# Kernel optimization log

Hardware: AMD Instinct MI355X
Metric: run time of the kernel (lower is better)

The kernel has to match this reference:

```python
import jax, jax.numpy as jnp
import numpy as np

N = 100000
E = 1600000
G = 64  # number of graphs
H = 128
BN_EPS = 1e-5


def setup_inputs() -> dict:
    key = jax.random.key(0)
    ks = jax.random.split(key, 12)
    x = jax.random.normal(ks[0], (N, 3), dtype=jnp.float32)
    edge_index = jax.random.randint(ks[1], (2, E), 0, N, dtype=jnp.int64)
    batch = jnp.sort(jax.random.randint(ks[2], (N,), 0, G, dtype=jnp.int64))
    W1 = jax.random.normal(ks[3], (3, H), dtype=jnp.float32) * 0.3
    W2 = jax.random.normal(ks[4], (H, H), dtype=jnp.float32) * 0.05
    W3 = jax.random.normal(ks[5], (H, H), dtype=jnp.float32) * 0.05
    lin_W = jax.random.normal(ks[6], (H, 2), dtype=jnp.float32) * 0.05
    d = {
        'x': x, 'edge_index': edge_index, 'batch': batch,
        'W1': W1, 'b1': jnp.zeros((H,), jnp.float32),
        'W2': W2, 'b2': jnp.zeros((H,), jnp.float32),
        'W3': W3, 'b3': jnp.zeros((H,), jnp.float32),
        'lin_W': lin_W, 'lin_b': jnp.zeros((2,), jnp.float32),
    }
    for i, kk in zip((1, 2, 3), ks[7:10]):
        d[f'bn{i}_g'] = jnp.ones((H,), jnp.float32)
        d[f'bn{i}_b'] = jnp.zeros((H,), jnp.float32)
        d[f'bn{i}_m'] = jnp.zeros((H,), jnp.float32)
        d[f'bn{i}_v'] = jax.random.uniform(kk, (H,), dtype=jnp.float32, minval=0.5, maxval=1.5)
    return d


def _gcn(x, src, dst, norm, W, b):
    # GCNConv: out = scatter_add(norm * (xW)[src], dst) + b
    h = x @ W
    msg = h[src] * norm[:, None]
    agg = jax.ops.segment_sum(msg, dst, num_segments=N)
    return agg + b


def _bn_eval(x, g, b, m, v):
    return (x - m) * jax.lax.rsqrt(v + BN_EPS) * g + b


def reference(x, edge_index, batch, W1, b1, W2, b2, W3, b3,
              bn1_g, bn1_b, bn1_m, bn1_v,
              bn2_g, bn2_b, bn2_m, bn2_v,
              bn3_g, bn3_b, bn3_m, bn3_v,
              lin_W, lin_b):
    loop = jnp.arange(N, dtype=edge_index.dtype)
    src = jnp.concatenate([edge_index[0], loop])
    dst = jnp.concatenate([edge_index[1], loop])
    # symmetric normalization with self-loops: deg from destination nodes
    deg = jax.ops.segment_sum(jnp.ones_like(dst, dtype=x.dtype), dst, num_segments=N)
    dinv = jnp.where(deg > 0, jax.lax.rsqrt(deg), 0.0)
    norm = dinv[src] * dinv[dst]

    h = jax.nn.relu(_bn_eval(_gcn(x, src, dst, norm, W1, b1), bn1_g, bn1_b, bn1_m, bn1_v))
    h = jax.nn.relu(_bn_eval(_gcn(h, src, dst, norm, W2, b2), bn2_g, bn2_b, bn2_m, bn2_v))
    h = jax.nn.relu(_bn_eval(_gcn(h, src, dst, norm, W3, b3), bn3_g, bn3_b, bn3_m, bn3_v))
    # dropout is identity in eval mode
    sums = jax.ops.segment_sum(h, batch, num_segments=G)
    cnts = jax.ops.segment_sum(jnp.ones((N,), h.dtype), batch, num_segments=G)
    pooled = sums / jnp.maximum(cnts, 1.0)[:, None]
    return pooled @ lin_W + lin_b
```

## Files before the change

### kernel.cpp

```cpp
#include <hip/hip_runtime.h>

#define NN 100000
#define EE 1600000
#define GG 64
#define HH 128
#define BN_EPS 1e-5f

#define CB 782
#define NB 256
#define TILE 6250

typedef unsigned short ushort_t;
typedef __attribute__((ext_vector_type(8))) short bf16x8;
typedef __attribute__((ext_vector_type(4))) float f32x4;

#define MFMA16 __builtin_amdgcn_mfma_f32_16x16x32_bf16

#define WFRAG_LO 16384

static __device__ inline ushort_t f2bf(float f) {
    unsigned u = __float_as_uint(f);
    unsigned r = (u + 0x7FFF + ((u >> 16) & 1)) >> 16;
    return (ushort_t)r;
}
static __device__ inline float bf2f(ushort_t b) {
    return __uint_as_float(((unsigned)b) << 16);
}


__global__ __launch_bounds__(256) void k_hist(const int* __restrict__ ei,
                                              int* __restrict__ histG) {
    __shared__ int h[CB];
    int t = threadIdx.x;
    for (int i = t; i < CB; i += 256) h[i] = 0;
    __syncthreads();
    int e0 = blockIdx.x * TILE;
    for (int i = t; i < TILE; i += 256) {
        int d = ei[EE + e0 + i];
        atomicAdd(&h[d >> 7], 1);
    }
    __syncthreads();
    for (int i = t; i < CB; i += 256) histG[blockIdx.x * CB + i] = h[i];
}

__global__ __launch_bounds__(NB) void k_bscan(int* __restrict__ histG,
                                              int* __restrict__ total) {
    __shared__ int sh[NB];
    int t = threadIdx.x;
    int c = blockIdx.x;
    sh[t] = histG[t * CB + c];
    __syncthreads();
    for (int d = 1; d < NB; d <<= 1) {
        int x = (t >= d) ? sh[t - d] : 0;
        __syncthreads();
        sh[t] += x;
        __syncthreads();
    }
    histG[t * CB + c] = (t > 0) ? sh[t - 1] : 0;
    if (t == NB - 1) total[c] = sh[NB - 1];
}

__global__ __launch_bounds__(1024) void k_cbase(const int* __restrict__ total,
                                                int* __restrict__ cbase) {
    __shared__ int sh[1024];
    int t = threadIdx.x;
    sh[t] = (t < CB) ? total[t] : 0;
    __syncthreads();
    for (int d = 1; d < 1024; d <<= 1) {
        int x = (t >= d) ? sh[t - d] : 0;
        __syncthreads();
        sh[t] += x;
        __syncthreads();
    }
    if (t < CB) cbase[t] = (t > 0) ? sh[t - 1] : 0;
    if (t == CB - 1) cbase[CB] = sh[t];
}

__global__ __launch_bounds__(256) void k_cscatter(const int* __restrict__ ei,
                                                  const int* __restrict__ histG,
                                                  const int* __restrict__ cbase,
                                                  int* __restrict__ metaS) {
    __shared__ int base_l[CB];
    __shared__ int cur_l[CB];
    int t = threadIdx.x;
    int b = blockIdx.x;
    for (int i = t; i < CB; i += 256) {
        base_l[i] = cbase[i] + histG[b * CB + i];
        cur_l[i] = 0;
    }
    __syncthreads();
    int e0 = b * TILE;
    for (int i = t; i < TILE; i += 256) {
        int s = ei[e0 + i];
        int d = ei[EE + e0 + i];
        int c = d >> 7;
        int p = base_l[c] + atomicAdd(&cur_l[c], 1);
        metaS[p] = s | ((d & 127) << 17);
    }
}

__global__ __launch_bounds__(256) void k_fine(const int* __restrict__ metaS,
                                              const int* __restrict__ cbase,
                                              int* __restrict__ cnt,
                                              int* __restrict__ offs,
                                              int* __restrict__ col,
                                              float* __restrict__ dinv) {
    __shared__ int hist[128];
    __shared__ int scn[128];
    __shared__ int cur[128];
    int t = threadIdx.x;
    int c = blockIdx.x;
    int lo = cbase[c], hi = cbase[c + 1];
    if (t < 128) hist[t] = 0;
    __syncthreads();
    for (int r = lo + t; r < hi; r += 256) atomicAdd(&hist[metaS[r] >> 17], 1);
    __syncthreads();
    if (t < 128) scn[t] = hist[t];
    __syncthreads();
    for (int d = 1; d < 128; d <<= 1) {
        int x = (t >= d && t < 128) ? scn[t - d] : 0;
        __syncthreads();
        if (t < 128) scn[t] += x;
        __syncthreads();
    }
    if (t < 128) {
        int excl = (t > 0) ? scn[t - 1] : 0;
        cur[t] = excl;
        int node = c * 128 + t;
        if (node < NN) {
            cnt[node] = hist[t];
            offs[node] = lo + excl;
            dinv[node] = rsqrtf((float)(hist[t] + 1));
        }
    }
    __syncthreads();
    for (int r = lo + t; r < hi; r += 256) {
        int pk = metaS[r];
        int s = pk & 0x1FFFF;
        int idx = atomicAdd(&cur[pk >> 17], 1);
        col[lo + idx] = s;
    }
}


__global__ __launch_bounds__(64) void k_gcnt(const int* __restrict__ batch,
                                             int* __restrict__ gcnt) {
    int g = threadIdx.x;
    int lo = 0, hi = NN;
    while (lo < hi) { int mid = (lo + hi) >> 1; if (batch[mid] < g) lo = mid + 1; else hi = mid; }
    int a = lo;
    lo = 0; hi = NN;
    int g1 = g + 1;
    while (lo < hi) { int mid = (lo + hi) >> 1; if (batch[mid] < g1) lo = mid + 1; else hi = mid; }
    gcnt[g] = lo - a;
}


__global__ __launch_bounds__(256) void k_wprep(const float* __restrict__ W2,
                                               const float* __restrict__ W3,
                                               ushort_t* __restrict__ w2f,
                                               ushort_t* __restrict__ w3f) {
    const float* W = (blockIdx.x & 8) ? W3 : W2;
    ushort_t* o = (blockIdx.x & 8) ? w3f : w2f;
    int tid = ((int)blockIdx.x & 7) * 256 + threadIdx.x;
    int l = tid & 63;
    int kb = ((tid >> 6) & 3) * 32 + (l >> 4) * 8;
    int n = (tid >> 8) * 16 + (l & 15);
    unsigned hp[4], lp[4];
#pragma unroll
    for (int p = 0; p < 4; p++) {
        float v0 = W[(size_t)(kb + 2 * p) * HH + n];
        float v1 = W[(size_t)(kb + 2 * p + 1) * HH + n];
        ushort_t h0 = f2bf(v0), h1 = f2bf(v1);
        ushort_t l0 = f2bf(v0 - bf2f(h0)), l1 = f2bf(v1 - bf2f(h1));
        hp[p] = (unsigned)h0 | ((unsigned)h1 << 16);
        lp[p] = (unsigned)l0 | ((unsigned)l1 << 16);
    }
    *(uint4*)&o[(size_t)tid * 8] = make_uint4(hp[0], hp[1], hp[2], hp[3]);
    *(uint4*)&o[WFRAG_LO + (size_t)tid * 8] = make_uint4(lp[0], lp[1], lp[2], lp[3]);
}


__global__ __launch_bounds__(256) void k_aggx(const float* __restrict__ x,
                                              const int* __restrict__ offs,
                                              const int* __restrict__ cnt,
                                              const int* __restrict__ col,
                                              const float* __restrict__ dinv,
                                              float* __restrict__ wgt,
                                              float4* __restrict__ agg) {
    int tid = threadIdx.x;
    int wave = tid >> 6;
    int lane = tid & 63;
    int grp = lane >> 4;
    int l = lane & 15;
    int n = blockIdx.x * 16 + wave * 4 + grp;
    float dv = dinv[n];
    int base = offs[n], cn = cnt[n];
    float a0 = 0.f, a1 = 0.f, a2 = 0.f;
    for (int i = l; i < cn; i += 16) {
        int s = col[base + i];
        float w = dinv[s] * dv;
        wgt[base + i] = w;
        a0 += w * x[s * 3 + 0];
        a1 += w * x[s * 3 + 1];
        a2 += w * x[s * 3 + 2];
    }
#pragma unroll
    for (int off = 8; off >= 1; off >>= 1) {
        a0 += __shfl_xor(a0, off, 16);
        a1 += __shfl_xor(a1, off, 16);
        a2 += __shfl_xor(a2, off, 16);
    }
    if (l == 0) {
        float w0 = dv * dv;
        a0 += w0 * x[n * 3 + 0];
        a1 += w0 * x[n * 3 + 1];
        a2 += w0 * x[n * 3 + 2];
        agg[n] = make_float4(a0, a1, a2, 0.f);
    }
}


__global__ __launch_bounds__(256) void k_mml1(const float4* __restrict__ agg,
                                              const float* __restrict__ W1,
                                              const float* __restrict__ b1,
                                              const float* __restrict__ g1,
                                              const float* __restrict__ bb1,
                                              const float* __restrict__ m1,
                                              const float* __restrict__ v1,
                                              const ushort_t* __restrict__ Wf,
                                              ushort_t* __restrict__ outB) {
    __shared__ float4 ag[64];
    __shared__ __align__(16) ushort_t xh[2][64 * HH];
    int tid = threadIdx.x;
    int row0 = blockIdx.x * 64;
    if (tid < 64) {
        int gr = row0 + tid;
        ag[tid] = (gr < NN) ? agg[gr] : make_float4(0.f, 0.f, 0.f, 0.f);
    }
    __syncthreads();
    {
        int c = tid & 127;
        int rh = tid >> 7;
        float w0 = W1[c], w1 = W1[128 + c], w2 = W1[256 + c];
        float sc = g1[c] * rsqrtf(v1[c] + BN_EPS);
        float sh = (b1[c] - m1[c]) * sc + bb1[c];
#pragma unroll
        for (int i = 0; i < 32; i++) {
            int r = 2 * i + rh;
            float4 a = ag[r];
            float t = fmaxf((a.x * w0 + a.y * w1 + a.z * w2) * sc + sh, 0.f);
            ushort_t hi = f2bf(t);
            ushort_t lo = f2bf(t - bf2f(hi));
            int idx = r * HH + (c ^ ((r & 7) << 3));
            xh[0][idx] = hi;
            xh[1][idx] = lo;
        }
    }
    __syncthreads();

    int w = tid >> 6, l = tid & 63;
    int r_lo = l & 15, kgrp = l >> 4;
    int row_l = w * 16 + r_lo;
    f32x4 acc[8];
#pragma unroll
    for (int nt = 0; nt < 8; nt++) acc[nt] = (f32x4){0.f, 0.f, 0.f, 0.f};

#pragma unroll
    for (int kk = 0; kk < 4; kk++) {
        int ke = kk * 32 + kgrp * 8;
        int idx = row_l * HH + (ke ^ ((row_l & 7) << 3));
        bf16x8 ahf = *(const bf16x8*)&xh[0][idx];
        bf16x8 alf = *(const bf16x8*)&xh[1][idx];
#pragma unroll
        for (int nt = 0; nt < 8; nt++) {
            int fo = ((((nt << 2) | kk) << 6) + l) * 8;
            bf16x8 bh = *(const bf16x8*)&Wf[fo];
            bf16x8 bl = *(const bf16x8*)&Wf[WFRAG_LO + fo];
            acc[nt] = MFMA16(ahf, bh, acc[nt], 0, 0, 0);
            acc[nt] = MFMA16(ahf, bl, acc[nt], 0, 0, 0);
            acc[nt] = MFMA16(alf, bh, acc[nt], 0, 0, 0);
        }
    }
#pragma unroll
    for (int q = 0; q < 4; q++) {
        int gr = row0 + w * 16 + kgrp * 4 + q;
        if (gr < NN) {
            size_t rb = (size_t)gr * HH + r_lo;
#pragma unroll
            for (int nt = 0; nt < 8; nt++)
                outB[rb + nt * 16] = f2bf(acc[nt][q]);
        }
    }
}


__global__ __launch_bounds__(256) void k_mm(const ushort_t* __restrict__ xin,
                                            const ushort_t* __restrict__ Wf,
                                            ushort_t* __restrict__ outB) {
    int tid = threadIdx.x;
    int w = tid >> 6, l = tid & 63;
    int row0 = blockIdx.x * 128 + w * 32;
    int r_lo = l & 15, kgrp = l >> 4;
    f32x4 acc[2][8];
#pragma unroll
    for (int rt = 0; rt < 2; rt++)
#pragma unroll
        for (int nt = 0; nt < 8; nt++) acc[rt][nt] = (f32x4){0.f, 0.f, 0.f, 0.f};

    bf16x8 za = {0, 0, 0, 0, 0, 0, 0, 0};
#pragma unroll
    for (int kk = 0; kk < 4; kk++) {
        int ke = kk * 32 + kgrp * 8;
        int ra0 = row0 + r_lo;
        int ra1 = row0 + 16 + r_lo;
        bf16x8 a0 = (ra0 < NN) ? *(const bf16x8*)&xin[(size_t)ra0 * HH + ke] : za;
        bf16x8 a1 = (ra1 < NN) ? *(const bf16x8*)&xin[(size_t)ra1 * HH + ke] : za;
#pragma unroll
        for (int nt = 0; nt < 8; nt++) {
            int fo = ((((nt << 2) | kk) << 6) + l) * 8;
            bf16x8 bh = *(const bf16x8*)&Wf[fo];
            bf16x8 bl = *(const bf16x8*)&Wf[WFRAG_LO + fo];
            acc[0][nt] = MFMA16(a0, bh, acc[0][nt], 0, 0, 0);
            acc[0][nt] = MFMA16(a0, bl, acc[0][nt], 0, 0, 0);
            acc[1][nt] = MFMA16(a1, bh, acc[1][nt], 0, 0, 0);
            acc[1][nt] = MFMA16(a1, bl, acc[1][nt], 0, 0, 0);
        }
    }
#pragma unroll
    for (int rt = 0; rt < 2; rt++)
#pragma unroll
        for (int q = 0; q < 4; q++) {
            int gr = row0 + rt * 16 + kgrp * 4 + q;
            if (gr < NN) {
                size_t rb = (size_t)gr * HH + r_lo;
#pragma unroll
                for (int nt = 0; nt < 8; nt++)
                    outB[rb + nt * 16] = f2bf(acc[rt][nt][q]);
            }
        }
}


__global__ __launch_bounds__(256) void k_agg(const ushort_t* __restrict__ t,
                                             const int* __restrict__ offs,
                                             const int* __restrict__ cnt,
                                             const int* __restrict__ col,
                                             const float* __restrict__ wgt,
                                             const float* __restrict__ dinv,
                                             const float* __restrict__ bias,
                                             const float* __restrict__ g,
                                             const float* __restrict__ bb,
                                             const float* __restrict__ m,
                                             const float* __restrict__ v,
                                             ushort_t* __restrict__ out) {
    int wave = threadIdx.x >> 6;
    int lane = threadIdx.x & 63;
    int half = lane >> 5;
    int l = lane & 31;
    int d = blockIdx.x * 8 + wave * 2 + half;
    int c0 = l * 4;
    float dv = dinv[d];
    float w0 = dv * dv;
    ushort4 selfR = *(const ushort4*)&t[(size_t)d * HH + c0];
    float4 acc;
    acc.x = bf2f(selfR.x) * w0; acc.y = bf2f(selfR.y) * w0;
    acc.z = bf2f(selfR.z) * w0; acc.w = bf2f(selfR.w) * w0;
    int base = offs[d], cn = cnt[d];
    for (int ib = 0; ib < cn; ib += 32) {
        int i = ib + l;
        int s = 0;
        float w = 0.f;
        if (i < cn) {
            s = col[base + i];
            w = wgt[base + i];
        }
        int lim = min(32, cn - ib);
#pragma unroll 8
        for (int j = 0; j < lim; j++) {
            int ss = __shfl(s, j, 32);
            float ww = __shfl(w, j, 32);
            ushort4 tv = *(const ushort4*)&t[(size_t)ss * HH + c0];
            acc.x += ww * bf2f(tv.x);
            acc.y += ww * bf2f(tv.y);
            acc.z += ww * bf2f(tv.z);
            acc.w += ww * bf2f(tv.w);
        }
    }
    float4 gg = *(const float4*)&g[c0];
    float4 vv = *(const float4*)&v[c0];
    float4 mm = *(const float4*)&m[c0];
    float4 bv = *(const float4*)&bb[c0];
    float4 bi = *(const float4*)&bias[c0];
    float sc0 = gg.x * rsqrtf(vv.x + BN_EPS);
    float sc1 = gg.y * rsqrtf(vv.y + BN_EPS);
    float sc2 = gg.z * rsqrtf(vv.z + BN_EPS);
    float sc3 = gg.w * rsqrtf(vv.w + BN_EPS);
    ushort4 o;
    o.x = f2bf(fmaxf(acc.x * sc0 + (bi.x - mm.x) * sc0 + bv.x, 0.f));
    o.y = f2bf(fmaxf(acc.y * sc1 + (bi.y - mm.y) * sc1 + bv.y, 0.f));
    o.z = f2bf(fmaxf(acc.z * sc2 + (bi.z - mm.z) * sc2 + bv.z, 0.f));
    o.w = f2bf(fmaxf(acc.w * sc3 + (bi.w - mm.w) * sc3 + bv.w, 0.f));
    *(ushort4*)&out[(size_t)d * HH + c0] = o;
}


#define PBLK 2048
__global__ void k_pool(const ushort_t* __restrict__ h, const int* __restrict__ batch,
                       float* __restrict__ gsum) {
    int c = threadIdx.x;
    int per = (NN + PBLK - 1) / PBLK;
    int n0 = blockIdx.x * per;
    int n1 = min(NN, n0 + per);
    if (n0 >= NN) return;
    float acc = 0.f;
    int cur = batch[n0];
    for (int n = n0; n < n1; n++) {
        int gr = batch[n];
        if (gr != cur) {
            atomicAdd(&gsum[cur * HH + c], acc);
            acc = 0.f; cur = gr;
        }
        acc += bf2f(h[(size_t)n * HH + c]);
    }
    atomicAdd(&gsum[cur * HH + c], acc);
}


__global__ void k_head(const float* __restrict__ gsum, const int* __restrict__ gcnt,
                       const float* __restrict__ linW, const float* __restrict__ linb,
                       float* __restrict__ out) {
    int t = threadIdx.x;
    int gr = t >> 1, j = t & 1;
    float inv = 1.0f / fmaxf((float)gcnt[gr], 1.0f);
    float acc = 0.f;
    for (int c = 0; c < HH; c++) acc += gsum[gr * HH + c] * linW[c * 2 + j];
    out[t] = acc * inv + linb[j];
}


static inline size_t al256(size_t x) { return (x + 255) & ~(size_t)255; }

extern "C" void kernel_launch(void* const* d_in, const int* in_sizes, int n_in,
                              void* d_out, int out_size, void* d_ws, size_t ws_size,
                              hipStream_t stream) {
    const float* x    = (const float*)d_in[0];
    const int*   ei   = (const int*)d_in[1];
    const int*   batch= (const int*)d_in[2];
    const float* W1   = (const float*)d_in[3];
    const float* b1   = (const float*)d_in[4];
    const float* W2   = (const float*)d_in[5];
    const float* b2   = (const float*)d_in[6];
    const float* W3   = (const float*)d_in[7];
    const float* b3   = (const float*)d_in[8];
    const float* linW = (const float*)d_in[9];
    const float* linb = (const float*)d_in[10];
    const float* bn1g = (const float*)d_in[11];
    const float* bn1b = (const float*)d_in[12];
    const float* bn1m = (const float*)d_in[13];
    const float* bn1v = (const float*)d_in[14];
    const float* bn2g = (const float*)d_in[15];
    const float* bn2b = (const float*)d_in[16];
    const float* bn2m = (const float*)d_in[17];
    const float* bn2v = (const float*)d_in[18];
    const float* bn3g = (const float*)d_in[19];
    const float* bn3b = (const float*)d_in[20];
    const float* bn3m = (const float*)d_in[21];
    const float* bn3v = (const float*)d_in[22];
    float* out = (float*)d_out;

    char* ws = (char*)d_ws;
    size_t off = 0;
    int*    histG  = (int*)(ws + off);    off += al256((size_t)NB * CB * 4);
    int*    total  = (int*)(ws + off);    off += al256((size_t)CB * 4);
    int*    cbase  = (int*)(ws + off);    off += al256((size_t)(CB + 1) * 4);
    int*    cnt    = (int*)(ws + off);    off += al256((size_t)NN * 4);
    int*    offs   = (int*)(ws + off);    off += al256((size_t)NN * 4);
    float*  dinv   = (float*)(ws + off);  off += al256((size_t)NN * 4);
    int*    col    = (int*)(ws + off);    off += al256((size_t)EE * 4);
    float*  wgt    = (float*)(ws + off);  off += al256((size_t)EE * 4);
    ushort_t* w2f  = (ushort_t*)(ws + off); off += al256((size_t)2 * WFRAG_LO * 2);
    ushort_t* w3f  = (ushort_t*)(ws + off); off += al256((size_t)2 * WFRAG_LO * 2);
    float4* agg    = (float4*)(ws + off); off += al256((size_t)NN * 16);
    char*   bufA   = (char*)(ws + off);   off += al256((size_t)NN * HH * 2);
    char*   bufB   = (char*)(ws + off);   off += al256((size_t)NN * HH * 4);
    float*  gsum   = (float*)(ws + off);  off += (size_t)GG * HH * 4;
    int*    gcnt   = (int*)(ws + off);    off += al256((size_t)GG * 4);

    int* metaS = (int*)bufB;
    ushort_t* tB = (ushort_t*)bufB;
    ushort_t* hB = (ushort_t*)bufA;

    hipMemsetAsync(gsum, 0, (size_t)GG * HH * 4, stream);

    k_wprep<<<16, 256, 0, stream>>>(W2, W3, w2f, w3f);
    k_gcnt<<<1, 64, 0, stream>>>(batch, gcnt);

    k_hist<<<NB, 256, 0, stream>>>(ei, histG);
    k_bscan<<<CB, NB, 0, stream>>>(histG, total);
    k_cbase<<<1, 1024, 0, stream>>>(total, cbase);
    k_cscatter<<<NB, 256, 0, stream>>>(ei, histG, cbase, metaS);
    k_fine<<<CB, 256, 0, stream>>>(metaS, cbase, cnt, offs, col, dinv);

    k_aggx<<<NN / 16, 256, 0, stream>>>(x, offs, cnt, col, dinv, wgt, agg);

    k_mml1<<<(NN + 63) / 64, 256, 0, stream>>>(agg, W1, b1, bn1g, bn1b, bn1m, bn1v,
                                               w2f, tB);
    k_agg<<<NN / 8, 256, 0, stream>>>(tB, offs, cnt, col, wgt, dinv,
                                      b2, bn2g, bn2b, bn2m, bn2v, hB);

    k_mm<<<(NN + 127) / 128, 256, 0, stream>>>(hB, w3f, tB);
    k_agg<<<NN / 8, 256, 0, stream>>>(tB, offs, cnt, col, wgt, dinv,
                                      b3, bn3g, bn3b, bn3m, bn3v, hB);

    k_pool<<<PBLK, 128, 0, stream>>>(hB, batch, gsum);
    k_head<<<1, 128, 0, stream>>>(gsum, gcnt, linW, linb, out);
}
```

Measured before the change: 403.0 us.

## Replace two-level bucketed CSR build with global atomic count, scan and scatter

Replaces the coarse-bucket histogram, block scans and fine per-bucket sort used to build the destination-sorted CSR with a simpler pipeline: global atomic degree counts, a three-kernel prefix scan, and an atomic-cursor scatter that also writes edge weights. It also pads x to float4 so the first aggregation does one vector gather per neighbor and reads precomputed weights. This removes several passes over the edge list and the metaS intermediate, but relies on many global atomics on random node counters, and neighbor order within each row becomes nondeterministic.

Result: slower. 527.2 us (+30.8%).

```diff
diff --git a/kernel.cpp b/kernel.cpp
--- a/kernel.cpp
+++ b/kernel.cpp
@@ -6,9 +6,8 @@
 #define HH 128
 #define BN_EPS 1e-5f
 
-#define CB 782
-#define NB 256
-#define TILE 6250
+#define SCB 1024
+#define SCN 98
 
 typedef unsigned short ushort_t;
 typedef __attribute__((ext_vector_type(8))) short bf16x8;
@@ -28,117 +27,74 @@
 }
 
 
-__global__ __launch_bounds__(256) void k_hist(const int* __restrict__ ei,
-                                              int* __restrict__ histG) {
-    __shared__ int h[CB];
+__global__ __launch_bounds__(256) void k_cnt(const int* __restrict__ ei,
+                                             int* __restrict__ cnt) {
+    int i = blockIdx.x * 256 + threadIdx.x;
+    int stride = gridDim.x * 256;
+    for (int e = i; e < EE; e += stride) atomicAdd(&cnt[ei[EE + e]], 1);
+}
+
+__global__ __launch_bounds__(SCB) void k_scanA(const int* __restrict__ cnt,
+                                               int* __restrict__ offs,
+                                               int* __restrict__ bsum) {
+    __shared__ int sh[SCB];
     int t = threadIdx.x;
-    for (int i = t; i < CB; i += 256) h[i] = 0;
+    int i = blockIdx.x * SCB + t;
+    int v = (i < NN) ? cnt[i] : 0;
+    sh[t] = v;
     __syncthreads();
-    int e0 = blockIdx.x * TILE;
-    for (int i = t; i < TILE; i += 256) {
-        int d = ei[EE + e0 + i];
-        atomicAdd(&h[d >> 7], 1);
-    }
-    __syncthreads();
-    for (int i = t; i < CB; i += 256) histG[blockIdx.x * CB + i] = h[i];
-}
-
-__global__ __launch_bounds__(NB) void k_bscan(int* __restrict__ histG,
-                                              int* __restrict__ total) {
-    __shared__ int sh[NB];
-    int t = threadIdx.x;
-    int c = blockIdx.x;
-    sh[t] = histG[t * CB + c];
-    __syncthreads();
-    for (int d = 1; d < NB; d <<= 1) {
+    for (int d = 1; d < SCB; d <<= 1) {
         int x = (t >= d) ? sh[t - d] : 0;
         __syncthreads();
         sh[t] += x;
         __syncthreads();
     }
-    histG[t * CB + c] = (t > 0) ? sh[t - 1] : 0;
-    if (t == NB - 1) total[c] = sh[NB - 1];
-}
-
-__global__ __launch_bounds__(1024) void k_cbase(const int* __restrict__ total,
-                                                int* __restrict__ cbase) {
-    __shared__ int sh[1024];
+    if (i < NN) offs[i] = sh[t] - v;
+    if (t == SCB - 1) bsum[blockIdx.x] = sh[t];
+}
+
+__global__ __launch_bounds__(128) void k_scanB(int* __restrict__ bsum) {
+    __shared__ int sh[128];
     int t = threadIdx.x;
-    sh[t] = (t < CB) ? total[t] : 0;
+    int v = (t < SCN) ? bsum[t] : 0;
+    sh[t] = v;
     __syncthreads();
-    for (int d = 1; d < 1024; d <<= 1) {
+    for (int d = 1; d < 128; d <<= 1) {
         int x = (t >= d) ? sh[t - d] : 0;
         __syncthreads();
         sh[t] += x;
         __syncthreads();
     }
-    if (t < CB) cbase[t] = (t > 0) ? sh[t - 1] : 0;
-    if (t == CB - 1) cbase[CB] = sh[t];
-}
-
-__global__ __launch_bounds__(256) void k_cscatter(const int* __restrict__ ei,
-                                                  const int* __restrict__ histG,
-                                                  const int* __restrict__ cbase,
-                                                  int* __restrict__ metaS) {
-    __shared__ int base_l[CB];
-    __shared__ int cur_l[CB];
-    int t = threadIdx.x;
-    int b = blockIdx.x;
-    for (int i = t; i < CB; i += 256) {
-        base_l[i] = cbase[i] + histG[b * CB + i];
-        cur_l[i] = 0;
-    }
-    __syncthreads();
-    int e0 = b * TILE;
-    for (int i = t; i < TILE; i += 256) {
-        int s = ei[e0 + i];
-        int d = ei[EE + e0 + i];
-        int c = d >> 7;
-        int p = base_l[c] + atomicAdd(&cur_l[c], 1);
-        metaS[p] = s | ((d & 127) << 17);
-    }
-}
-
-__global__ __launch_bounds__(256) void k_fine(const int* __restrict__ metaS,
-                                              const int* __restrict__ cbase,
-                                              int* __restrict__ cnt,
-                                              int* __restrict__ offs,
-                                              int* __restrict__ col,
-                                              float* __restrict__ dinv) {
-    __shared__ int hist[128];
-    __shared__ int scn[128];
-    __shared__ int cur[128];
-    int t = threadIdx.x;
-    int c = blockIdx.x;
-    int lo = cbase[c], hi = cbase[c + 1];
-    if (t < 128) hist[t] = 0;
-    __syncthreads();
-    for (int r = lo + t; r < hi; r += 256) atomicAdd(&hist[metaS[r] >> 17], 1);
-    __syncthreads();
-    if (t < 128) scn[t] = hist[t];
-    __syncthreads();
-    for (int d = 1; d < 128; d <<= 1) {
-        int x = (t >= d && t < 128) ? scn[t - d] : 0;
-        __syncthreads();
-        if (t < 128) scn[t] += x;
-        __syncthreads();
-    }
-    if (t < 128) {
-        int excl = (t > 0) ? scn[t - 1] : 0;
-        cur[t] = excl;
-        int node = c * 128 + t;
-        if (node < NN) {
-            cnt[node] = hist[t];
-            offs[node] = lo + excl;
-            dinv[node] = rsqrtf((float)(hist[t] + 1));
-        }
-    }
-    __syncthreads();
-    for (int r = lo + t; r < hi; r += 256) {
-        int pk = metaS[r];
-        int s = pk & 0x1FFFF;
-        int idx = atomicAdd(&cur[pk >> 17], 1);
-        col[lo + idx] = s;
+    if (t < SCN) bsum[t] = sh[t] - v;
+}
+
+__global__ __launch_bounds__(SCB) void k_scanC(const int* __restrict__ cnt,
+                                               const int* __restrict__ bsum,
+                                               int* __restrict__ offs,
+                                               int* __restrict__ cur,
+                                               float* __restrict__ dinv) {
+    int i = blockIdx.x * SCB + threadIdx.x;
+    if (i < NN) {
+        int o = offs[i] + bsum[blockIdx.x];
+        offs[i] = o;
+        cur[i] = o;
+        dinv[i] = rsqrtf((float)(cnt[i] + 1));
+    }
+}
+
+__global__ __launch_bounds__(256) void k_scatter(const int* __restrict__ ei,
+                                                 const float* __restrict__ dinv,
+                                                 int* __restrict__ cur,
+                                                 int* __restrict__ col,
+                                                 float* __restrict__ wgt) {
+    int i = blockIdx.x * 256 + threadIdx.x;
+    int stride = gridDim.x * 256;
+    for (int e = i; e < EE; e += stride) {
+        int s = ei[e];
+        int d = ei[EE + e];
+        int p = atomicAdd(&cur[d], 1);
+        col[p] = s;
+        wgt[p] = dinv[s] * dinv[d];
     }
 }
 
@@ -181,12 +137,19 @@
 }
 
 
-__global__ __launch_bounds__(256) void k_aggx(const float* __restrict__ x,
+__global__ __launch_bounds__(256) void k_xpad(const float* __restrict__ x,
+                                              float4* __restrict__ xp) {
+    int i = blockIdx.x * 256 + threadIdx.x;
+    if (i < NN) xp[i] = make_float4(x[i * 3], x[i * 3 + 1], x[i * 3 + 2], 0.f);
+}
+
+
+__global__ __launch_bounds__(256) void k_aggx(const float4* __restrict__ xp,
                                               const int* __restrict__ offs,
                                               const int* __restrict__ cnt,
                                               const int* __restrict__ col,
+                                              const float* __restrict__ wgt,
                                               const float* __restrict__ dinv,
-                                              float* __restrict__ wgt,
                                               float4* __restrict__ agg) {
     int tid = threadIdx.x;
     int wave = tid >> 6;
@@ -199,11 +162,11 @@
     float a0 = 0.f, a1 = 0.f, a2 = 0.f;
     for (int i = l; i < cn; i += 16) {
         int s = col[base + i];
-        float w = dinv[s] * dv;
-        wgt[base + i] = w;
-        a0 += w * x[s * 3 + 0];
-        a1 += w * x[s * 3 + 1];
-        a2 += w * x[s * 3 + 2];
+        float w = wgt[base + i];
+        float4 xv = xp[s];
+        a0 += w * xv.x;
+        a1 += w * xv.y;
+        a2 += w * xv.z;
     }
 #pragma unroll
     for (int off = 8; off >= 1; off >>= 1) {
@@ -213,9 +176,10 @@
     }
     if (l == 0) {
         float w0 = dv * dv;
-        a0 += w0 * x[n * 3 + 0];
-        a1 += w0 * x[n * 3 + 1];
-        a2 += w0 * x[n * 3 + 2];
+        float4 xv = xp[n];
+        a0 += w0 * xv.x;
+        a1 += w0 * xv.y;
+        a2 += w0 * xv.z;
         agg[n] = make_float4(a0, a1, a2, 0.f);
     }
 }
@@ -471,38 +435,39 @@
 
     char* ws = (char*)d_ws;
     size_t off = 0;
-    int*    histG  = (int*)(ws + off);    off += al256((size_t)NB * CB * 4);
-    int*    total  = (int*)(ws + off);    off += al256((size_t)CB * 4);
-    int*    cbase  = (int*)(ws + off);    off += al256((size_t)(CB + 1) * 4);
     int*    cnt    = (int*)(ws + off);    off += al256((size_t)NN * 4);
     int*    offs   = (int*)(ws + off);    off += al256((size_t)NN * 4);
+    int*    cur    = (int*)(ws + off);    off += al256((size_t)NN * 4);
+    int*    bsum   = (int*)(ws + off);    off += al256((size_t)128 * 4);
     float*  dinv   = (float*)(ws + off);  off += al256((size_t)NN * 4);
     int*    col    = (int*)(ws + off);    off += al256((size_t)EE * 4);
     float*  wgt    = (float*)(ws + off);  off += al256((size_t)EE * 4);
     ushort_t* w2f  = (ushort_t*)(ws + off); off += al256((size_t)2 * WFRAG_LO * 2);
     ushort_t* w3f  = (ushort_t*)(ws + off); off += al256((size_t)2 * WFRAG_LO * 2);
+    float4* xp     = (float4*)(ws + off); off += al256((size_t)NN * 16);
     float4* agg    = (float4*)(ws + off); off += al256((size_t)NN * 16);
     char*   bufA   = (char*)(ws + off);   off += al256((size_t)NN * HH * 2);
     char*   bufB   = (char*)(ws + off);   off += al256((size_t)NN * HH * 4);
     float*  gsum   = (float*)(ws + off);  off += (size_t)GG * HH * 4;
     int*    gcnt   = (int*)(ws + off);    off += al256((size_t)GG * 4);
 
-    int* metaS = (int*)bufB;
     ushort_t* tB = (ushort_t*)bufB;
     ushort_t* hB = (ushort_t*)bufA;
 
     hipMemsetAsync(gsum, 0, (size_t)GG * HH * 4, stream);
+    hipMemsetAsync(cnt, 0, (size_t)NN * 4, stream);
 
     k_wprep<<<16, 256, 0, stream>>>(W2, W3, w2f, w3f);
     k_gcnt<<<1, 64, 0, stream>>>(batch, gcnt);
-
-    k_hist<<<NB, 256, 0, stream>>>(ei, histG);
-    k_bscan<<<CB, NB, 0, stream>>>(histG, total);
-    k_cbase<<<1, 1024, 0, stream>>>(total, cbase);
-    k_cscatter<<<NB, 256, 0, stream>>>(ei, histG, cbase, metaS);
-    k_fine<<<CB, 256, 0, stream>>>(metaS, cbase, cnt, offs, col, dinv);
-
-    k_aggx<<<NN / 16, 256, 0, stream>>>(x, offs, cnt, col, dinv, wgt, agg);
+    k_xpad<<<(NN + 255) / 256, 256, 0, stream>>>(x, xp);
+
+    k_cnt<<<2048, 256, 0, stream>>>(ei, cnt);
+    k_scanA<<<SCN, SCB, 0, stream>>>(cnt, offs, bsum);
+    k_scanB<<<1, 128, 0, stream>>>(bsum);
+    k_scanC<<<SCN, SCB, 0, stream>>>(cnt, bsum, offs, cur, dinv);
+    k_scatter<<<2048, 256, 0, stream>>>(ei, dinv, cur, col, wgt);
+
+    k_aggx<<<NN / 16, 256, 0, stream>>>(xp, offs, cnt, col, wgt, dinv, agg);
 
     k_mml1<<<(NN + 63) / 64, 256, 0, stream>>>(agg, W1, b1, bn1g, bn1b, bn1m, bn1v,
                                                w2f, tB);
```
